# Kernel tuning notes

Measured on AMD Instinct MI355X. Metric: run time of the kernel, lower is better.

Reference implementation:

```python
import jax, jax.numpy as jnp
import numpy as np

B, N, ND, HD = 8, 512, 128, 256
NUM_OPS, NUM_PARAMS = 64, 16


def setup_inputs() -> dict:
    key = jax.random.key(0)
    ks = iter(jax.random.split(key, 80))
    def nrm(shape, s=0.02):
        return jax.random.normal(next(ks), shape, dtype=jnp.float32) * s
    inp = {}
    inp['node_features'] = jax.random.normal(next(ks), (B, N, ND), dtype=jnp.float32)
    inp['adjacency'] = (jax.random.uniform(next(ks), (B, N, N)) < 0.1).astype(jnp.float32)
    inp['mask'] = jnp.ones((B, N), jnp.float32)
    inp['op_types'] = jnp.zeros((B, N, NUM_OPS), jnp.int32)  # only its shape is used (T = N)
    # GNN layer params: linear (out,in)+bias, attention linear (1, 2*out)+bias
    for i, ind in zip((1, 2, 3), (ND, HD, HD)):
        inp[f'g{i}_w'] = nrm((HD, ind)); inp[f'g{i}_b'] = nrm((HD,))
        inp[f'g{i}_aw'] = nrm((1, 2 * HD)); inp[f'g{i}_ab'] = nrm((1,))
    # 2-layer bidirectional LSTM; single fused bias (= b_ih + b_hh), gate order i,f,g,o
    for l, ind in ((0, HD), (1, 2 * HD)):
        for d in 'fb':
            inp[f'wih{l}{d}'] = nrm((4 * HD, ind))
            inp[f'whh{l}{d}'] = nrm((4 * HD, HD))
            inp[f'b{l}{d}'] = nrm((4 * HD,))
    # MLP heads (dropout is identity in eval)
    for name, outd in (('op', NUM_OPS), ('pp', NUM_PARAMS), ('sk', 128), ('nd', ND)):
        ind = HD if name == 'nd' else 2 * HD
        inp[f'{name}_w1'] = nrm((HD, ind)); inp[f'{name}_b1'] = nrm((HD,))
        inp[f'{name}_w2'] = nrm((outd, HD)); inp[f'{name}_b2'] = nrm((outd,))
    return inp


def gnn(x, adj, mask, w, b, aw, ab):
    # Faithful to: sigmoid(Linear(cat[h_i, h_j])) — factored as per-node projections
    h = x @ w.T + b                      # (B,N,D)
    D = h.shape[-1]
    si = h @ aw[0, :D] + ab[0]           # (B,N) row contribution (+bias once)
    sj = h @ aw[0, D:]                   # (B,N) col contribution
    score = jax.nn.sigmoid(si[:, :, None] + sj[:, None, :])  # (B,N,N)
    score = score * adj * mask[:, :, None] * mask[:, None, :]
    w_att = score / (score.sum(-1, keepdims=True) + 1e-8)
    return jnp.einsum('bij,bjd->bid', w_att, h) * mask[:, :, None]


def lstm_dir(x, wih, whh, b, reverse):
    # x: (B,T,In); returns (B,T,H), outputs aligned with input positions
    xs = jnp.swapaxes(x, 0, 1)
    Bc, H = x.shape[0], whh.shape[1]
    pre = xs @ wih.T + b                 # (T,B,4H) input projection hoisted out of scan
    def step(carry, p):
        h, c = carry
        g = p + h @ whh.T
        i, f, gg, o = jnp.split(g, 4, -1)
        c = jax.nn.sigmoid(f) * c + jax.nn.sigmoid(i) * jnp.tanh(gg)
        h = jax.nn.sigmoid(o) * jnp.tanh(c)
        return (h, c), h
    init = (jnp.zeros((Bc, H), x.dtype), jnp.zeros((Bc, H), x.dtype))
    _, ys = jax.lax.scan(step, init, pre, reverse=reverse)
    return jnp.swapaxes(ys, 0, 1)


def bidir(x, wf, hf, bf, wb, hb, bb):
    return jnp.concatenate([lstm_dir(x, wf, hf, bf, False),
                            lstm_dir(x, wb, hb, bb, True)], -1)


def mlp(x, w1, b1, w2, b2):
    return jax.nn.relu(x @ w1.T + b1) @ w2.T + b2


def reference(node_features, adjacency, mask, op_types,
              g1_w, g1_b, g1_aw, g1_ab, g2_w, g2_b, g2_aw, g2_ab,
              g3_w, g3_b, g3_aw, g3_ab,
              wih0f, whh0f, b0f, wih0b, whh0b, b0b,
              wih1f, whh1f, b1f, wih1b, whh1b, b1b,
              op_w1, op_b1, op_w2, op_b2, pp_w1, pp_b1, pp_w2, pp_b2,
              sk_w1, sk_b1, sk_w2, sk_b2, nd_w1, nd_b1, nd_w2, nd_b2):
    h = jax.nn.relu(gnn(node_features, adjacency, mask, g1_w, g1_b, g1_aw, g1_ab))
    h = jax.nn.relu(gnn(h, adjacency, mask, g2_w, g2_b, g2_aw, g2_ab))
    h = gnn(h, adjacency, mask, g3_w, g3_b, g3_aw, g3_ab)
    # mask is all-ones -> pack_padded_sequence == plain full-length LSTM, T == N
    x = bidir(h, wih0f, whh0f, b0f, wih0b, whh0b, b0b)
    x = bidir(x, wih1f, whh1f, b1f, wih1b, whh1b, b1b)
    op_pred = mlp(x, op_w1, op_b1, op_w2, op_b2)
    param_pred = mlp(x, pp_w1, pp_b1, pp_w2, pp_b2)
    sketch_pred = mlp(x, sk_w1, sk_b1, sk_w2, sk_b2)
    node_pred = mlp(h, nd_w1, nd_b1, nd_w2, nd_b2)
    return op_pred, param_pred, sketch_pred, node_pred
```

## Files before the change

### kernel.cpp

```cpp
#include <hip/hip_runtime.h>

#define BB   8
#define NN   512
#define NDIM 128
#define HDIM 256
#define TT   512

__device__ __forceinline__ float sigmoidf_(float x) { return 1.0f / (1.0f + __expf(-x)); }
__device__ __forceinline__ float tanhf_(float x) { float e = __expf(2.0f * x); return 1.0f - 2.0f / (e + 1.0f); }

typedef _Float16 half2v __attribute__((ext_vector_type(2)));
typedef unsigned int uint4v __attribute__((ext_vector_type(4)));
__device__ __forceinline__ float fdot2_(unsigned int w, unsigned int h, float acc) {
    return __builtin_amdgcn_fdot2(__builtin_bit_cast(half2v, w),
                                  __builtin_bit_cast(half2v, h), acc, false);
}

template<int RELU>
__global__ __launch_bounds__(256) void gemm_nt(const float* __restrict__ X,
    const float* __restrict__ W, const float* __restrict__ bias,
    float* __restrict__ Y, int M, int K, int Nn)
{
    __shared__ float Xs[16][68];
    __shared__ float Ws[16][68];
    const int tid = threadIdx.x;
    const int m0 = blockIdx.y << 6;
    const int n0 = blockIdx.x << 6;
    const int lr = tid >> 2;
    const int lc = (tid & 3) << 2;
    const int tm = (tid >> 4) << 2;
    const int tn = (tid & 15) << 2;

    float acc[4][4] = {{0.f,0.f,0.f,0.f},{0.f,0.f,0.f,0.f},{0.f,0.f,0.f,0.f},{0.f,0.f,0.f,0.f}};

    const float* Xp = X + (size_t)(m0 + lr) * K + lc;
    const bool wok = (n0 + lr) < Nn;
    const float* Wp = wok ? (W + (size_t)(n0 + lr) * K + lc) : W;

    for (int k0 = 0; k0 < K; k0 += 16) {
        float4 xv = *(const float4*)(Xp + k0);
        float4 wv = *(const float4*)(Wp + k0);
        if (!wok) wv = make_float4(0.f, 0.f, 0.f, 0.f);
        __syncthreads();
        Xs[lc+0][lr]=xv.x; Xs[lc+1][lr]=xv.y; Xs[lc+2][lr]=xv.z; Xs[lc+3][lr]=xv.w;
        Ws[lc+0][lr]=wv.x; Ws[lc+1][lr]=wv.y; Ws[lc+2][lr]=wv.z; Ws[lc+3][lr]=wv.w;
        __syncthreads();
        #pragma unroll
        for (int kk = 0; kk < 16; ++kk) {
            const float4 a = *(const float4*)(&Xs[kk][tm]);
            const float4 b = *(const float4*)(&Ws[kk][tn]);
            acc[0][0] += a.x*b.x; acc[0][1] += a.x*b.y; acc[0][2] += a.x*b.z; acc[0][3] += a.x*b.w;
            acc[1][0] += a.y*b.x; acc[1][1] += a.y*b.y; acc[1][2] += a.y*b.z; acc[1][3] += a.y*b.w;
            acc[2][0] += a.z*b.x; acc[2][1] += a.z*b.y; acc[2][2] += a.z*b.z; acc[2][3] += a.z*b.w;
            acc[3][0] += a.w*b.x; acc[3][1] += a.w*b.y; acc[3][2] += a.w*b.z; acc[3][3] += a.w*b.w;
        }
    }
    const int nc = n0 + tn;
    if (nc >= Nn) return;
    float4 bv = make_float4(0.f, 0.f, 0.f, 0.f);
    if (bias) bv = *(const float4*)(bias + nc);
    #pragma unroll
    for (int i = 0; i < 4; ++i) {
        float4 o;
        o.x = acc[i][0] + bv.x; o.y = acc[i][1] + bv.y;
        o.z = acc[i][2] + bv.z; o.w = acc[i][3] + bv.w;
        if (RELU) { o.x=fmaxf(o.x,0.f); o.y=fmaxf(o.y,0.f); o.z=fmaxf(o.z,0.f); o.w=fmaxf(o.w,0.f); }
        *(float4*)(Y + (size_t)(m0 + tm + i) * Nn + nc) = o;
    }
}

template<int RELU>
__global__ __launch_bounds__(256) void gemm_nn_mask(const float* __restrict__ A,
    const float* __restrict__ Hm, const float* __restrict__ mask,
    float* __restrict__ Y, int M, int K, int Nn)
{
    const int b = blockIdx.z;
    A  += (size_t)b * M * K;
    Hm += (size_t)b * K * Nn;
    Y  += (size_t)b * M * Nn;
    __shared__ float As[16][68];
    __shared__ float Hs[16][68];
    const int tid = threadIdx.x;
    const int m0 = blockIdx.y << 6;
    const int n0 = blockIdx.x << 6;
    const int lr = tid >> 2;
    const int lc = (tid & 3) << 2;
    const int hr = tid >> 4;
    const int hc = (tid & 15) << 2;
    const int tm = (tid >> 4) << 2;
    const int tn = (tid & 15) << 2;

    float acc[4][4] = {{0.f,0.f,0.f,0.f},{0.f,0.f,0.f,0.f},{0.f,0.f,0.f,0.f},{0.f,0.f,0.f,0.f}};

    for (int k0 = 0; k0 < K; k0 += 16) {
        float4 av = *(const float4*)(A + (size_t)(m0 + lr) * K + k0 + lc);
        float4 hv = *(const float4*)(Hm + (size_t)(k0 + hr) * Nn + n0 + hc);
        __syncthreads();
        As[lc+0][lr]=av.x; As[lc+1][lr]=av.y; As[lc+2][lr]=av.z; As[lc+3][lr]=av.w;
        *(float4*)(&Hs[hr][hc]) = hv;
        __syncthreads();
        #pragma unroll
        for (int kk = 0; kk < 16; ++kk) {
            const float4 a = *(const float4*)(&As[kk][tm]);
            const float4 h = *(const float4*)(&Hs[kk][tn]);
            acc[0][0] += a.x*h.x; acc[0][1] += a.x*h.y; acc[0][2] += a.x*h.z; acc[0][3] += a.x*h.w;
            acc[1][0] += a.y*h.x; acc[1][1] += a.y*h.y; acc[1][2] += a.y*h.z; acc[1][3] += a.y*h.w;
            acc[2][0] += a.z*h.x; acc[2][1] += a.z*h.y; acc[2][2] += a.z*h.z; acc[2][3] += a.z*h.w;
            acc[3][0] += a.w*h.x; acc[3][1] += a.w*h.y; acc[3][2] += a.w*h.z; acc[3][3] += a.w*h.w;
        }
    }
    #pragma unroll
    for (int i = 0; i < 4; ++i) {
        const float mk = mask[b * M + m0 + tm + i];
        float4 o;
        o.x = acc[i][0]*mk; o.y = acc[i][1]*mk; o.z = acc[i][2]*mk; o.w = acc[i][3]*mk;
        if (RELU) { o.x=fmaxf(o.x,0.f); o.y=fmaxf(o.y,0.f); o.z=fmaxf(o.z,0.f); o.w=fmaxf(o.w,0.f); }
        *(float4*)(Y + (size_t)(m0 + tm + i) * Nn + n0 + tn) = o;
    }
}

__global__ __launch_bounds__(256) void attn_sisj(const float* __restrict__ h,
    const float* __restrict__ aw, const float* __restrict__ ab,
    float* __restrict__ si, float* __restrict__ sj)
{
    const int lane = threadIdx.x & 63;
    const int row  = (blockIdx.x << 2) + (threadIdx.x >> 6);
    const float4 hv = ((const float4*)(h + (size_t)row * HDIM))[lane];
    const float4 a1 = ((const float4*)aw)[lane];
    const float4 a2 = ((const float4*)(aw + HDIM))[lane];
    float s1 = hv.x*a1.x + hv.y*a1.y + hv.z*a1.z + hv.w*a1.w;
    float s2 = hv.x*a2.x + hv.y*a2.y + hv.z*a2.z + hv.w*a2.w;
    #pragma unroll
    for (int off = 32; off > 0; off >>= 1) {
        s1 += __shfl_down(s1, off);
        s2 += __shfl_down(s2, off);
    }
    if (lane == 0) { si[row] = s1 + ab[0]; sj[row] = s2; }
}

__global__ __launch_bounds__(512) void attn_score(const float* __restrict__ si,
    const float* __restrict__ sj, const float* __restrict__ adj,
    const float* __restrict__ mask, float* __restrict__ watt)
{
    const int bi = blockIdx.x;
    const int b  = bi >> 9;
    const int j  = threadIdx.x;
    const float s0 = si[bi];
    const float mi = mask[bi];
    float s = sigmoidf_(s0 + sj[(b << 9) + j]) * adj[(size_t)bi * NN + j] * mi * mask[(b << 9) + j];
    float t = s;
    #pragma unroll
    for (int off = 32; off > 0; off >>= 1) t += __shfl_down(t, off);
    __shared__ float red[8];
    const int lane = j & 63, wv = j >> 6;
    if (lane == 0) red[wv] = t;
    __syncthreads();
    if (j == 0) {
        float tot = 0.f;
        #pragma unroll
        for (int w = 0; w < 8; ++w) tot += red[w];
        red[0] = 1.0f / (tot + 1e-8f);
    }
    __syncthreads();
    watt[(size_t)bi * NN + j] = s * red[0];
}

__global__ __launch_bounds__(256) void pack_f16(const float* __restrict__ src,
    unsigned int* __restrict__ dst, int n)
{
    int i = blockIdx.x * 256 + threadIdx.x;
    if (i < n) {
        float2 v = ((const float2*)src)[i];
        _Float16 a = (_Float16)v.x, b = (_Float16)v.y;
        unsigned short ua = *(unsigned short*)&a, ub = *(unsigned short*)&b;
        dst[i] = (unsigned int)ua | ((unsigned int)ub << 16);
    }
}

__global__ __launch_bounds__(1024) __attribute__((amdgpu_waves_per_eu(4, 4)))
void lstm_scan7(
    const float* __restrict__ pre_f, const float* __restrict__ pre_b,
    const unsigned int* __restrict__ w16_f, const unsigned int* __restrict__ w16_b,
    float* __restrict__ out)
{
    __shared__ uint4v lw4[8 * 1024];
    __shared__ float g_s[1024];
    __shared__ unsigned int h2[128];

    const int chain = blockIdx.x;
    const int batch = chain >> 1;
    const int dir   = chain & 1;
    const float* pre = dir ? pre_b : pre_f;
    const unsigned int* w = dir ? w16_b : w16_f;
    const int t0 = threadIdx.x;

    const uint4v* wr = (const uint4v*)(w + (size_t)t0 * 128);

    #pragma unroll
    for (int i = 0; i < 8; ++i) lw4[i * 1024 + t0] = wr[24 + i];

#define WD(i) uint4v W##i = wr[i];
    WD(0) WD(1) WD(2) WD(3) WD(4) WD(5) WD(6) WD(7) WD(8) WD(9) WD(10) WD(11)
    WD(12) WD(13) WD(14) WD(15) WD(16) WD(17) WD(18) WD(19) WD(20) WD(21) WD(22) WD(23)
#undef WD
#define PIN_ALL \
    { \
        asm volatile("" : "+v"(W0)); asm volatile("" : "+v"(W1)); \
        asm volatile("" : "+v"(W2)); asm volatile("" : "+v"(W3)); \
        asm volatile("" : "+v"(W4)); asm volatile("" : "+v"(W5)); \
        asm volatile("" : "+v"(W6)); asm volatile("" : "+v"(W7)); \
        asm volatile("" : "+v"(W8)); asm volatile("" : "+v"(W9)); \
        asm volatile("" : "+v"(W10)); asm volatile("" : "+v"(W11)); \
        asm volatile("" : "+v"(W12)); asm volatile("" : "+v"(W13)); \
        asm volatile("" : "+v"(W14)); asm volatile("" : "+v"(W15)); \
        asm volatile("" : "+v"(W16)); asm volatile("" : "+v"(W17)); \
        asm volatile("" : "+v"(W18)); asm volatile("" : "+v"(W19)); \
        asm volatile("" : "+v"(W20)); asm volatile("" : "+v"(W21)); \
        asm volatile("" : "+v"(W22)); asm volatile("" : "+v"(W23)); \
    }
    PIN_ALL

    if (t0 < 128) h2[t0] = 0u;
    float c = 0.f;

    const int tt0 = dir ? (TT - 1) : 0;
    const long pstep = dir ? -1024 : 1024;
    const long ostep = dir ? -512 : 512;
    const float* pp = pre + ((size_t)batch * TT + tt0) * 1024 + t0;
    float* op = out + ((size_t)batch * TT + tt0) * 512 + dir * 256 + t0;
    float pv = *pp; pp += pstep;
    __syncthreads();

    for (int t = 0; t < TT; ++t) {
        PIN_ALL

        float pv_n = 0.f;
        if (t + 1 < TT) pv_n = *pp;
        pp += pstep;

        float a0 = 0.f, a1 = 0.f, a2 = 0.f, a3 = 0.f;
        const uint4v* h4 = (const uint4v*)h2;
#define DOT(i) { const uint4v hv = h4[i]; \
        a0 = fdot2_(W##i.x, hv.x, a0); a1 = fdot2_(W##i.y, hv.y, a1); \
        a2 = fdot2_(W##i.z, hv.z, a2); a3 = fdot2_(W##i.w, hv.w, a3); }
        DOT(0) DOT(1) DOT(2) DOT(3) DOT(4) DOT(5) DOT(6) DOT(7)
        DOT(8) DOT(9) DOT(10) DOT(11) DOT(12) DOT(13) DOT(14) DOT(15)
        DOT(16) DOT(17) DOT(18) DOT(19) DOT(20) DOT(21) DOT(22) DOT(23)
#undef DOT
        #pragma unroll
        for (int i = 0; i < 8; ++i) {
            const uint4v wv = lw4[i * 1024 + t0];
            const uint4v hv = h4[24 + i];
            a0 = fdot2_(wv.x, hv.x, a0); a1 = fdot2_(wv.y, hv.y, a1);
            a2 = fdot2_(wv.z, hv.z, a2); a3 = fdot2_(wv.w, hv.w, a3);
        }
        g_s[t0] = (a0 + a1) + (a2 + a3) + pv;
        __syncthreads();
        if (t0 < 256) {
            const float ig = sigmoidf_(g_s[t0]);
            const float fg = sigmoidf_(g_s[256 + t0]);
            const float gg = tanhf_(g_s[512 + t0]);
            const float og = sigmoidf_(g_s[768 + t0]);
            c = fg * c + ig * gg;
            const float h = og * tanhf_(c);
            *op = h;
            op += ostep;
            _Float16 hh = (_Float16)h;
            ((unsigned short*)h2)[t0] = *(unsigned short*)&hh;
        }
        pv = pv_n;
        __syncthreads();
    }
#undef PIN_ALL
}


extern "C" void kernel_launch(void* const* d_in, const int* in_sizes, int n_in,
                              void* d_out, int out_size, void* d_ws, size_t ws_size,
                              hipStream_t stream)
{
    const float* nf   = (const float*)d_in[0];
    const float* adj  = (const float*)d_in[1];
    const float* mask = (const float*)d_in[2];
    const float* g_w[3]  = {(const float*)d_in[4],  (const float*)d_in[8],  (const float*)d_in[12]};
    const float* g_b[3]  = {(const float*)d_in[5],  (const float*)d_in[9],  (const float*)d_in[13]};
    const float* g_aw[3] = {(const float*)d_in[6],  (const float*)d_in[10], (const float*)d_in[14]};
    const float* g_ab[3] = {(const float*)d_in[7],  (const float*)d_in[11], (const float*)d_in[15]};
    const float* wih0f = (const float*)d_in[16]; const float* whh0f = (const float*)d_in[17]; const float* b0f = (const float*)d_in[18];
    const float* wih0b = (const float*)d_in[19]; const float* whh0b = (const float*)d_in[20]; const float* b0b = (const float*)d_in[21];
    const float* wih1f = (const float*)d_in[22]; const float* whh1f = (const float*)d_in[23]; const float* b1f = (const float*)d_in[24];
    const float* wih1b = (const float*)d_in[25]; const float* whh1b = (const float*)d_in[26]; const float* b1b = (const float*)d_in[27];

    float* ws = (float*)d_ws;
    float* bufA = ws;
    float* bufB = bufA + 1048576;
    float* bufC = bufB + 1048576;
    float* si   = bufC + 1048576;
    float* sj   = si + 4096;
    float* out0 = sj + 4096;
    float* out1 = out0 + 2097152;
    float* P0   = out1 + 2097152;
    float* P1   = P0 + 4194304;
    float* watt = P0;
    unsigned int* w16_0f = (unsigned int*)bufB;
    unsigned int* w16_0b = w16_0f + 131072;
    unsigned int* w16_1f = w16_0b + 131072;
    unsigned int* w16_1b = w16_1f + 131072;

    const int MR = BB * NN;
    dim3 blk(256);

    auto run_gnn = [&](const float* xin, int Kin, int li, float* ob, bool relu) {
        gemm_nt<0><<<dim3(HDIM / 64, MR / 64), blk, 0, stream>>>(xin, g_w[li], g_b[li], bufA, MR, Kin, HDIM);
        attn_sisj<<<dim3(MR / 4), blk, 0, stream>>>(bufA, g_aw[li], g_ab[li], si, sj);
        attn_score<<<dim3(MR), dim3(512), 0, stream>>>(si, sj, adj, mask, watt);
        if (relu)
            gemm_nn_mask<1><<<dim3(HDIM / 64, NN / 64, BB), blk, 0, stream>>>(watt, bufA, mask, ob, NN, NN, HDIM);
        else
            gemm_nn_mask<0><<<dim3(HDIM / 64, NN / 64, BB), blk, 0, stream>>>(watt, bufA, mask, ob, NN, NN, HDIM);
    };
    run_gnn(nf,   NDIM, 0, bufB, true);
    run_gnn(bufB, HDIM, 1, bufB, true);
    run_gnn(bufB, HDIM, 2, bufC, false);

    pack_f16<<<dim3(512), blk, 0, stream>>>(whh0f, w16_0f, 131072);
    pack_f16<<<dim3(512), blk, 0, stream>>>(whh0b, w16_0b, 131072);
    pack_f16<<<dim3(512), blk, 0, stream>>>(whh1f, w16_1f, 131072);
    pack_f16<<<dim3(512), blk, 0, stream>>>(whh1b, w16_1b, 131072);

    gemm_nt<0><<<dim3(16, MR / 64), blk, 0, stream>>>(bufC, wih0f, b0f, P0, MR, HDIM, 1024);
    gemm_nt<0><<<dim3(16, MR / 64), blk, 0, stream>>>(bufC, wih0b, b0b, P1, MR, HDIM, 1024);
    lstm_scan7<<<dim3(16), dim3(1024), 0, stream>>>(P0, P1, w16_0f, w16_0b, out0);

    gemm_nt<0><<<dim3(16, MR / 64), blk, 0, stream>>>(out0, wih1f, b1f, P0, MR, 512, 1024);
    gemm_nt<0><<<dim3(16, MR / 64), blk, 0, stream>>>(out0, wih1b, b1b, P1, MR, 512, 1024);
    lstm_scan7<<<dim3(16), dim3(1024), 0, stream>>>(P0, P1, w16_1f, w16_1b, out1);

    float* out = (float*)d_out;
    gemm_nt<1><<<dim3(4, MR / 64), blk, 0, stream>>>(out1, (const float*)d_in[28], (const float*)d_in[29], bufA, MR, 512, 256);
    gemm_nt<0><<<dim3(1, MR / 64), blk, 0, stream>>>(bufA, (const float*)d_in[30], (const float*)d_in[31], out, MR, 256, 64);
    gemm_nt<1><<<dim3(4, MR / 64), blk, 0, stream>>>(out1, (const float*)d_in[32], (const float*)d_in[33], bufA, MR, 512, 256);
    gemm_nt<0><<<dim3(1, MR / 64), blk, 0, stream>>>(bufA, (const float*)d_in[34], (const float*)d_in[35], out + 262144, MR, 256, 16);
    gemm_nt<1><<<dim3(4, MR / 64), blk, 0, stream>>>(out1, (const float*)d_in[36], (const float*)d_in[37], bufA, MR, 512, 256);
    gemm_nt<0><<<dim3(2, MR / 64), blk, 0, stream>>>(bufA, (const float*)d_in[38], (const float*)d_in[39], out + 327680, MR, 256, 128);
    gemm_nt<1><<<dim3(4, MR / 64), blk, 0, stream>>>(bufC, (const float*)d_in[40], (const float*)d_in[41], bufA, MR, 256, 256);
    gemm_nt<0><<<dim3(2, MR / 64), blk, 0, stream>>>(bufA, (const float*)d_in[42], (const float*)d_in[43], out + 851968, MR, 256, 128);
}
```

Before: 2.543 ms.

## Move dense projection GEMMs to bf16 MFMA with pre-packed operands

Adds a 128x128-tile bf16 MFMA GEMM kernel and a pack kernel that converts activations and weights to bf16. The GNN projections, LSTM input projections and MLP first layers now run on matrix cores instead of FP32 FMA loops. The cost is extra pack passes over activations and weights, workspace aliasing of packed buffers, and reduced input precision (bf16) for these GEMMs. The LSTM scan and the attention kernels are unchanged, and the serial scan likely dominates total time.

```diff
diff --git a/kernel.cpp b/kernel.cpp
--- a/kernel.cpp
+++ b/kernel.cpp
@@ -11,9 +11,15 @@
 
 typedef _Float16 half2v __attribute__((ext_vector_type(2)));
 typedef unsigned int uint4v __attribute__((ext_vector_type(4)));
+typedef short bf16x8 __attribute__((ext_vector_type(8)));
+typedef float f32x4 __attribute__((ext_vector_type(4)));
 __device__ __forceinline__ float fdot2_(unsigned int w, unsigned int h, float acc) {
     return __builtin_amdgcn_fdot2(__builtin_bit_cast(half2v, w),
                                   __builtin_bit_cast(half2v, h), acc, false);
+}
+__device__ __forceinline__ unsigned short f2bf_(float x) {
+    unsigned int u = __builtin_bit_cast(unsigned int, x);
+    return (unsigned short)((u + 0x7FFFu + ((u >> 16) & 1u)) >> 16);
 }
 
 template<int RELU>
@@ -66,6 +72,68 @@
         o.z = acc[i][2] + bv.z; o.w = acc[i][3] + bv.w;
         if (RELU) { o.x=fmaxf(o.x,0.f); o.y=fmaxf(o.y,0.f); o.z=fmaxf(o.z,0.f); o.w=fmaxf(o.w,0.f); }
         *(float4*)(Y + (size_t)(m0 + tm + i) * Nn + nc) = o;
+    }
+}
+
+template<int RELU>
+__global__ __launch_bounds__(256) void gemm_nt_mfma(
+    const unsigned short* __restrict__ X, const unsigned short* __restrict__ W,
+    const float* __restrict__ bias, float* __restrict__ Y, int K, int Nn)
+{
+    __shared__ unsigned short As[128][56];
+    __shared__ unsigned short Bs[128][56];
+    const int tid = threadIdx.x;
+    const int m0 = blockIdx.y << 7;
+    const int n0 = blockIdx.x << 7;
+    const int wid = tid >> 6, lane = tid & 63;
+    const int wm = (wid >> 1) << 6;
+    const int wn = (wid & 1) << 6;
+    const int sr = tid >> 2;
+    const int sc = (tid & 3) << 3;
+
+    f32x4 acc[4][4] = {};
+
+    const int fr = lane & 15;
+    const int kg = (lane >> 4) << 3;
+
+    for (int k0 = 0; k0 < K; k0 += 32) {
+        uint4 a0 = *(const uint4*)(X + (size_t)(m0 + sr) * K + k0 + sc);
+        uint4 a1 = *(const uint4*)(X + (size_t)(m0 + sr + 64) * K + k0 + sc);
+        uint4 b0 = *(const uint4*)(W + (size_t)(n0 + sr) * K + k0 + sc);
+        uint4 b1 = *(const uint4*)(W + (size_t)(n0 + sr + 64) * K + k0 + sc);
+        __syncthreads();
+        *(uint4*)&As[sr][sc] = a0; *(uint4*)&As[sr + 64][sc] = a1;
+        *(uint4*)&Bs[sr][sc] = b0; *(uint4*)&Bs[sr + 64][sc] = b1;
+        __syncthreads();
+        bf16x8 af[4], bf[4];
+        #pragma unroll
+        for (int i = 0; i < 4; ++i) {
+            af[i] = *(const bf16x8*)&As[wm + i * 16 + fr][kg];
+            bf[i] = *(const bf16x8*)&Bs[wn + i * 16 + fr][kg];
+        }
+        #pragma unroll
+        for (int i = 0; i < 4; ++i)
+            #pragma unroll
+            for (int j = 0; j < 4; ++j)
+                acc[i][j] = __builtin_amdgcn_mfma_f32_16x16x32_bf16(af[i], bf[j], acc[i][j], 0, 0, 0);
+    }
+
+    const int cr = (lane >> 4) << 2;
+    const int cc = lane & 15;
+    #pragma unroll
+    for (int i = 0; i < 4; ++i) {
+        #pragma unroll
+        for (int j = 0; j < 4; ++j) {
+            const int col = n0 + wn + j * 16 + cc;
+            const float bv = bias ? bias[col] : 0.f;
+            #pragma unroll
+            for (int r = 0; r < 4; ++r) {
+                const int row = m0 + wm + i * 16 + cr + r;
+                float v = acc[i][j][r] + bv;
+                if (RELU) v = fmaxf(v, 0.f);
+                Y[(size_t)row * Nn + col] = v;
+            }
+        }
     }
 }
 
@@ -175,6 +243,23 @@
         unsigned short ua = *(unsigned short*)&a, ub = *(unsigned short*)&b;
         dst[i] = (unsigned int)ua | ((unsigned int)ub << 16);
     }
+}
+
+__global__ __launch_bounds__(256) void pack3_bf16(
+    const float* __restrict__ s0, unsigned short* __restrict__ d0, int n0,
+    const float* __restrict__ s1, unsigned short* __restrict__ d1, int n1,
+    const float* __restrict__ s2, unsigned short* __restrict__ d2, int n2)
+{
+    int i = (blockIdx.x * 256 + threadIdx.x) * 4;
+    const float* s; unsigned short* d; int l;
+    if (i < n0) { s = s0; d = d0; l = i; }
+    else if (i < n0 + n1) { s = s1; d = d1; l = i - n0; }
+    else if (i < n0 + n1 + n2) { s = s2; d = d2; l = i - n0 - n1; }
+    else return;
+    float4 v = *(const float4*)(s + l);
+    ushort4 o;
+    o.x = f2bf_(v.x); o.y = f2bf_(v.y); o.z = f2bf_(v.z); o.w = f2bf_(v.w);
+    *(ushort4*)(d + l) = o;
 }
 
 __global__ __launch_bounds__(1024) __attribute__((amdgpu_waves_per_eu(4, 4)))
@@ -306,12 +391,31 @@
     unsigned int* w16_0b = w16_0f + 131072;
     unsigned int* w16_1f = w16_0b + 131072;
     unsigned int* w16_1b = w16_1f + 131072;
+    unsigned short* nfp   = (unsigned short*)P1;
+    unsigned short* bufBp = (unsigned short*)(P1 + 262144);
+    unsigned short* gwp1  = (unsigned short*)(P1 + 786432);
+    unsigned short* gwp2  = (unsigned short*)(P1 + 802816);
+    unsigned short* gwp3  = (unsigned short*)(P1 + 835584);
+    unsigned short* bufCp  = (unsigned short*)bufA;
+    unsigned short* out0p  = (unsigned short*)bufA;
+    unsigned short* wih0fp = (unsigned short*)out1;
+    unsigned short* wih0bp = (unsigned short*)(out1 + 131072);
+    unsigned short* wih1fp = (unsigned short*)(out1 + 262144);
+    unsigned short* wih1bp = (unsigned short*)(out1 + 524288);
+    unsigned short* out1p  = (unsigned short*)P0;
+    unsigned short* bufCp2 = (unsigned short*)(P0 + 1048576);
+    unsigned short* opw1p  = (unsigned short*)(P0 + 1572864);
+    unsigned short* ppw1p  = (unsigned short*)(P0 + 1638400);
+    unsigned short* skw1p  = (unsigned short*)(P0 + 1703936);
+    unsigned short* ndw1p  = (unsigned short*)(P0 + 1769472);
 
     const int MR = BB * NN;
     dim3 blk(256);
 
-    auto run_gnn = [&](const float* xin, int Kin, int li, float* ob, bool relu) {
-        gemm_nt<0><<<dim3(HDIM / 64, MR / 64), blk, 0, stream>>>(xin, g_w[li], g_b[li], bufA, MR, Kin, HDIM);
+    pack3_bf16<<<dim3(608), blk, 0, stream>>>(nf, nfp, 524288,
+                                              g_w[0], gwp1, 32768,
+                                              g_w[1], gwp2, 65536);
+    auto run_attn = [&](int li, float* ob, bool relu) {
         attn_sisj<<<dim3(MR / 4), blk, 0, stream>>>(bufA, g_aw[li], g_ab[li], si, sj);
         attn_score<<<dim3(MR), dim3(512), 0, stream>>>(si, sj, adj, mask, watt);
         if (relu)
@@ -319,30 +423,51 @@
         else
             gemm_nn_mask<0><<<dim3(HDIM / 64, NN / 64, BB), blk, 0, stream>>>(watt, bufA, mask, ob, NN, NN, HDIM);
     };
-    run_gnn(nf,   NDIM, 0, bufB, true);
-    run_gnn(bufB, HDIM, 1, bufB, true);
-    run_gnn(bufB, HDIM, 2, bufC, false);
+    gemm_nt_mfma<0><<<dim3(2, 32), blk, 0, stream>>>(nfp, gwp1, g_b[0], bufA, NDIM, HDIM);
+    run_attn(0, bufB, true);
+    pack3_bf16<<<dim3(1088), blk, 0, stream>>>(bufB, bufBp, 1048576,
+                                               g_w[2], gwp3, 65536,
+                                               (const float*)0, (unsigned short*)0, 0);
+    gemm_nt_mfma<0><<<dim3(2, 32), blk, 0, stream>>>(bufBp, gwp2, g_b[1], bufA, HDIM, HDIM);
+    run_attn(1, bufB, true);
+    pack3_bf16<<<dim3(1024), blk, 0, stream>>>(bufB, bufBp, 1048576,
+                                               (const float*)0, (unsigned short*)0, 0,
+                                               (const float*)0, (unsigned short*)0, 0);
+    gemm_nt_mfma<0><<<dim3(2, 32), blk, 0, stream>>>(bufBp, gwp3, g_b[2], bufA, HDIM, HDIM);
+    run_attn(2, bufC, false);
 
     pack_f16<<<dim3(512), blk, 0, stream>>>(whh0f, w16_0f, 131072);
     pack_f16<<<dim3(512), blk, 0, stream>>>(whh0b, w16_0b, 131072);
     pack_f16<<<dim3(512), blk, 0, stream>>>(whh1f, w16_1f, 131072);
     pack_f16<<<dim3(512), blk, 0, stream>>>(whh1b, w16_1b, 131072);
 
-    gemm_nt<0><<<dim3(16, MR / 64), blk, 0, stream>>>(bufC, wih0f, b0f, P0, MR, HDIM, 1024);
-    gemm_nt<0><<<dim3(16, MR / 64), blk, 0, stream>>>(bufC, wih0b, b0b, P1, MR, HDIM, 1024);
+    pack3_bf16<<<dim3(1536), blk, 0, stream>>>(bufC, bufCp, 1048576,
+                                               wih0f, wih0fp, 262144,
+                                               wih0b, wih0bp, 262144);
+    gemm_nt_mfma<0><<<dim3(8, 32), blk, 0, stream>>>(bufCp, wih0fp, b0f, P0, HDIM, 1024);
+    gemm_nt_mfma<0><<<dim3(8, 32), blk, 0, stream>>>(bufCp, wih0bp, b0b, P1, HDIM, 1024);
     lstm_scan7<<<dim3(16), dim3(1024), 0, stream>>>(P0, P1, w16_0f, w16_0b, out0);
 
-    gemm_nt<0><<<dim3(16, MR / 64), blk, 0, stream>>>(out0, wih1f, b1f, P0, MR, 512, 1024);
-    gemm_nt<0><<<dim3(16, MR / 64), blk, 0, stream>>>(out0, wih1b, b1b, P1, MR, 512, 1024);
+    pack3_bf16<<<dim3(3072), blk, 0, stream>>>(out0, out0p, 2097152,
+                                               wih1f, wih1fp, 524288,
+                                               wih1b, wih1bp, 524288);
+    gemm_nt_mfma<0><<<dim3(8, 32), blk, 0, stream>>>(out0p, wih1fp, b1f, P0, 512, 1024);
+    gemm_nt_mfma<0><<<dim3(8, 32), blk, 0, stream>>>(out0p, wih1bp, b1b, P1, 512, 1024);
     lstm_scan7<<<dim3(16), dim3(1024), 0, stream>>>(P0, P1, w16_1f, w16_1b, out1);
 
     float* out = (float*)d_out;
-    gemm_nt<1><<<dim3(4, MR / 64), blk, 0, stream>>>(out1, (const float*)d_in[28], (const float*)d_in[29], bufA, MR, 512, 256);
+    pack3_bf16<<<dim3(3200), blk, 0, stream>>>(out1, out1p, 2097152,
+                                               bufC, bufCp2, 1048576,
+                                               (const float*)d_in[28], opw1p, 131072);
+    pack3_bf16<<<dim3(320), blk, 0, stream>>>((const float*)d_in[32], ppw1p, 131072,
+                                              (const float*)d_in[36], skw1p, 131072,
+                                              (const float*)d_in[40], ndw1p, 65536);
+    gemm_nt_mfma<1><<<dim3(2, 32), blk, 0, stream>>>(out1p, opw1p, (const float*)d_in[29], bufA, 512, 256);
     gemm_nt<0><<<dim3(1, MR / 64), blk, 0, stream>>>(bufA, (const float*)d_in[30], (const float*)d_in[31], out, MR, 256, 64);
-    gemm_nt<1><<<dim3(4, MR / 64), blk, 0, stream>>>(out1, (const float*)d_in[32], (const float*)d_in[33], bufA, MR, 512, 256);
+    gemm_nt_mfma<1><<<dim3(2, 32), blk, 0, stream>>>(out1p, ppw1p, (const float*)d_in[33], bufA, 512, 256);
     gemm_nt<0><<<dim3(1, MR / 64), blk, 0, stream>>>(bufA, (const float*)d_in[34], (const float*)d_in[35], out + 262144, MR, 256, 16);
-    gemm_nt<1><<<dim3(4, MR / 64), blk, 0, stream>>>(out1, (const float*)d_in[36], (const float*)d_in[37], bufA, MR, 512, 256);
+    gemm_nt_mfma<1><<<dim3(2, 32), blk, 0, stream>>>(out1p, skw1p, (const float*)d_in[37], bufA, 512, 256);
     gemm_nt<0><<<dim3(2, MR / 64), blk, 0, stream>>>(bufA, (const float*)d_in[38], (const float*)d_in[39], out + 327680, MR, 256, 128);
-    gemm_nt<1><<<dim3(4, MR / 64), blk, 0, stream>>>(bufC, (const float*)d_in[40], (const float*)d_in[41], bufA, MR, 256, 256);
+    gemm_nt_mfma<1><<<dim3(2, 32), blk, 0, stream>>>(bufCp2, ndw1p, (const float*)d_in[41], bufA, 256, 256);
     gemm_nt<0><<<dim3(2, MR / 64), blk, 0, stream>>>(bufA, (const float*)d_in[42], (const float*)d_in[43], out + 851968, MR, 256, 128);
 }
```

Result: faster. 2.365 ms (-7.0%).
